# Optimization experiments

Hardware: AMD Instinct MI355X
Metric: run time of the kernel (lower is better)

## Reference

```python
import jax, jax.numpy as jnp
import numpy as np

D = 4096
H = 4 * D
EPS = 1e-5


def layer_norm(x, g, b):
    mu = jnp.mean(x, axis=-1, keepdims=True)
    var = jnp.mean(jnp.square(x - mu), axis=-1, keepdims=True)
    return (x - mu) * jax.lax.rsqrt(var + EPS) * g + b


def setup_inputs() -> dict:
    key = jax.random.key(0)
    ks = jax.random.split(key, 8)
    s = 0.02
    return {
        "x": jax.random.normal(ks[0], (2, 2048, D), dtype=jnp.float32),
        "Wq": jax.random.normal(ks[1], (D, D), dtype=jnp.float32) * s,
        "bq": jnp.zeros((D,), jnp.float32),
        "Wk": jax.random.normal(ks[2], (D, D), dtype=jnp.float32) * s,
        "bk": jnp.zeros((D,), jnp.float32),
        "Wv": jax.random.normal(ks[3], (D, D), dtype=jnp.float32) * s,
        "bv": jnp.zeros((D,), jnp.float32),
        "Wo": jax.random.normal(ks[4], (D, D), dtype=jnp.float32) * s,
        "bo": jnp.zeros((D,), jnp.float32),
        "g1": jnp.ones((D,), jnp.float32),
        "b1": jnp.zeros((D,), jnp.float32),
        "g2": jnp.ones((D,), jnp.float32),
        "b2": jnp.zeros((D,), jnp.float32),
        "W1": jax.random.normal(ks[5], (D, H), dtype=jnp.float32) * s,
        "bi1": jnp.zeros((H,), jnp.float32),
        "W2": jax.random.normal(ks[6], (H, D), dtype=jnp.float32) * s,
        "bi2": jnp.zeros((D,), jnp.float32),
    }


def reference(x, Wq, bq, Wk, bk, Wv, bv, Wo, bo, g1, b1, g2, b2, W1, bi1, W2, bi2):
    # single-head attention, scale = sqrt(D) (as in the source)
    Q = x @ Wq + bq          # [B, S, D]
    K = x @ Wk + bk
    V = x @ Wv + bv
    scores = jnp.einsum("bsd,btd->bst", Q, K) / jnp.sqrt(jnp.float32(D))
    attn = jax.nn.softmax(scores, axis=-1) @ V   # [B, S, D]
    x = attn @ Wo + bo + x
    x = layer_norm(x, g1, b1)
    h = jax.nn.gelu(x @ W1 + bi1, approximate=False)  # torch nn.GELU default = exact erf
    x = h @ W2 + bi2 + x
    x = layer_norm(x, g2, b2)
    return x
```

## Files before the change

kernel.cpp:

```cpp
#include <hip/hip_runtime.h>
#include <hip/hip_bf16.h>

typedef __bf16 bf16x8 __attribute__((ext_vector_type(8)));
typedef float  f32x4  __attribute__((ext_vector_type(4)));
typedef unsigned short u16;
typedef unsigned int   u32;

#define DEV __device__ __forceinline__

DEV u16 f2bu(float f){ union{float f; u32 i;} x; x.f=f; u32 r=x.i+0x7FFFu+((x.i>>16)&1u); return (u16)(r>>16); }
DEV u32 pack2(float a, float b){ return (u32)f2bu(a) | ((u32)f2bu(b)<<16); }

DEV void gload16(const u16* g, u16* l){
  __builtin_amdgcn_global_load_lds((const __attribute__((address_space(1))) void*)g,
                                   (__attribute__((address_space(3))) void*)l, 16, 0, 0);
}

template<int BIAS, int GELU, int RESF32, int OUTF32>
__global__ __launch_bounds__(512, 2) void gemm256(
    const u16* __restrict__ A, const u16* __restrict__ Bt,
    const float* __restrict__ bias, const float* __restrict__ resid,
    float* __restrict__ outF, u16* __restrict__ outB,
    int M, int N, int K, int SWZ,
    long long sA, long long sB, long long sC)
{
  __shared__ __align__(16) u16 As[4][8192];
  __shared__ __align__(16) u16 Bs[4][8192];

  const int tid  = threadIdx.x;
  const int lane = tid & 63;
  const int wave = tid >> 6;
  const int wm = wave >> 2;
  const int wn = wave & 3;

  int bx = blockIdx.x, by = blockIdx.y;
  if (SWZ) {
    const int gx = gridDim.x;
    const int nwg = gx * gridDim.y;
    const int flat = by * gx + bx;
    const int cpx = nwg >> 3;
    const int s = (flat & 7) * cpx + (flat >> 3);
    bx = s % gx; by = s / gx;
  }
  const int rowBase = by * 256;
  const int colBase = bx * 256;

  const u16* Ag = A + (size_t)blockIdx.z * sA + (size_t)rowBase * K;
  const u16* Bg = Bt + (size_t)blockIdx.z * sB + (size_t)colBase * K;

  const int qsw = (lane & 3) ^ ((lane >> 3) & 3);
  const u16* apA0 = Ag + (size_t)(wave*32 + (lane>>2)) * K + qsw*8;
  const u16* apA1 = apA0 + (size_t)16 * K;
  const u16* apB0 = Bg + (size_t)(wave*32 + (lane>>2)) * K + qsw*8;
  const u16* apB1 = apB0 + (size_t)16 * K;
  u16* dA0 = &As[0][wave*1024 + lane*8];
  u16* dA1 = dA0 + 512;
  u16* dB0 = &Bs[0][wave*1024 + lane*8];
  u16* dB1 = dB0 + 512;

#define STAGE(t) { const int _b = (t) & 3; const size_t _k = (size_t)(t) * 32;          \
    gload16(apA0 + _k, dA0 + _b*8192); gload16(apA1 + _k, dA1 + _b*8192);               \
    gload16(apB0 + _k, dB0 + _b*8192); gload16(apB1 + _k, dB1 + _b*8192); }

  const int r15 = lane & 15;
  const int gp  = (lane >> 4) ^ ((lane >> 1) & 3);
  const u16* rdA = &As[0][(wm*128 + r15)*32 + gp*8];
  const u16* rdB = &Bs[0][(wn*64  + r15)*32 + gp*8];

  f32x4 acc[8][4];
  const f32x4 fz = {0.f,0.f,0.f,0.f};
#pragma unroll
  for (int m=0;m<8;++m)
#pragma unroll
    for (int n=0;n<4;++n) acc[m][n] = fz;

  const int KT = K >> 5;
  STAGE(0);
  if (KT > 1) STAGE(1);
  if (KT > 2) STAGE(2);

  for (int t = 0; t < KT; ++t) {
    const int rem = KT - t;
    if (rem > 2)      asm volatile("s_waitcnt vmcnt(8)" ::: "memory");
    else if (rem > 1) asm volatile("s_waitcnt vmcnt(4)" ::: "memory");
    else              asm volatile("s_waitcnt vmcnt(0)" ::: "memory");
    __builtin_amdgcn_s_barrier();
    asm volatile("" ::: "memory");

    const u16* pa = rdA + (t & 3) * 8192;
    const u16* pb = rdB + (t & 3) * 8192;
    bf16x8 a[8], b[4];
#pragma unroll
    for (int m=0;m<8;++m) a[m] = *(const bf16x8*)(pa + m*512);
#pragma unroll
    for (int n=0;n<4;++n) b[n] = *(const bf16x8*)(pb + n*512);

    if (t + 3 < KT) STAGE(t + 3);

    __builtin_amdgcn_s_setprio(1);
#pragma unroll
    for (int m=0;m<8;++m)
#pragma unroll
      for (int n=0;n<4;++n)
        acc[m][n] = __builtin_amdgcn_mfma_f32_16x16x32_bf16(a[m], b[n], acc[m][n], 0,0,0);
    __builtin_amdgcn_s_setprio(0);
  }
#undef STAGE

  const long long cb = (long long)blockIdx.z * sC;
  const int q4 = (lane >> 4) * 4;
#pragma unroll
  for (int m=0;m<8;++m){
    const int row0 = rowBase + wm*128 + m*16 + q4;
#pragma unroll
    for (int n=0;n<4;++n){
      const int col = colBase + wn*64 + n*16 + r15;
      float bb = 0.f;
      if (BIAS) bb = bias[col];
#pragma unroll
      for (int r=0;r<4;++r){
        float v = acc[m][n][r] + bb;
        if (GELU) v = 0.5f*v*(1.f+erff(v*0.70710678118654752f));
        const size_t oi = (size_t)cb + (size_t)(row0+r)*N + col;
        if (RESF32) v += resid[oi];
        if (OUTF32) outF[oi] = v;
        else        outB[oi] = f2bu(v);
      }
    }
  }
}

__global__ __launch_bounds__(256) void tr_f32_bf16(
    const float* __restrict__ in, u16* __restrict__ out, int R, int C)
{
  __shared__ float tile[64][65];
  const int t = threadIdx.x;
  const int tr = blockIdx.y*64, tc = blockIdx.x*64;
  const int c4 = (t&15)*4;
#pragma unroll
  for (int i=0;i<4;++i){
    const int r = i*16 + (t>>4);
    const float4 v = *reinterpret_cast<const float4*>(&in[(size_t)(tr+r)*C + tc + c4]);
    tile[r][c4+0]=v.x; tile[r][c4+1]=v.y; tile[r][c4+2]=v.z; tile[r][c4+3]=v.w;
  }
  __syncthreads();
#pragma unroll
  for (int i=0;i<4;++i){
    const int c = i*16 + (t>>4);
    uint2 o;
    o.x = pack2(tile[c4+0][c], tile[c4+1][c]);
    o.y = pack2(tile[c4+2][c], tile[c4+3][c]);
    *reinterpret_cast<uint2*>(&out[(size_t)(tc+c)*R + tr + c4]) = o;
  }
}

__global__ __launch_bounds__(256) void tr_bf16(
    const u16* __restrict__ in, u16* __restrict__ out, int R, int C,
    long long sIn, long long sOut)
{
  __shared__ u16 tile[64][72];
  const long long z = blockIdx.z;
  in  += z*sIn; out += z*sOut;
  const int t = threadIdx.x;
  const int tr = blockIdx.y*64, tc = blockIdx.x*64;
  const int c4 = (t&15)*4;
#pragma unroll
  for (int i=0;i<4;++i){
    const int r = i*16 + (t>>4);
    const uint2 v = *reinterpret_cast<const uint2*>(&in[(size_t)(tr+r)*C + tc + c4]);
    tile[r][c4+0]=(u16)(v.x&0xffffu); tile[r][c4+1]=(u16)(v.x>>16);
    tile[r][c4+2]=(u16)(v.y&0xffffu); tile[r][c4+3]=(u16)(v.y>>16);
  }
  __syncthreads();
#pragma unroll
  for (int i=0;i<4;++i){
    const int c = i*16 + (t>>4);
    uint2 o;
    o.x = (u32)tile[c4+0][c] | ((u32)tile[c4+1][c]<<16);
    o.y = (u32)tile[c4+2][c] | ((u32)tile[c4+3][c]<<16);
    *reinterpret_cast<uint2*>(&out[(size_t)(tc+c)*R + tr + c4]) = o;
  }
}

__global__ __launch_bounds__(256) void cvt_f32_bf16(
    const float* __restrict__ in, u16* __restrict__ out, int n4)
{
  const int i = blockIdx.x*256 + threadIdx.x;
  if (i >= n4) return;
  const float4 v = reinterpret_cast<const float4*>(in)[i];
  uint2 o; o.x = pack2(v.x,v.y); o.y = pack2(v.z,v.w);
  reinterpret_cast<uint2*>(out)[i] = o;
}

__global__ __launch_bounds__(256) void softmax2048(
    const float* __restrict__ S, u16* __restrict__ P, float scale)
{
  const size_t row = blockIdx.x;
  const float4* src = reinterpret_cast<const float4*>(S + row*2048);
  const int t = threadIdx.x, lane = t&63, wave = t>>6;
  const float4 a = src[t], b = src[t+256];
  float v[8] = {a.x,a.y,a.z,a.w,b.x,b.y,b.z,b.w};
  float m = -3.4e38f;
#pragma unroll
  for (int i=0;i<8;++i){ v[i]*=scale; m = fmaxf(m, v[i]); }
#pragma unroll
  for (int o=32;o>0;o>>=1) m = fmaxf(m, __shfl_xor(m, o));
  __shared__ float red[8];
  if (lane==0) red[wave]=m;
  __syncthreads();
  m = fmaxf(fmaxf(red[0],red[1]), fmaxf(red[2],red[3]));
  float s = 0.f;
#pragma unroll
  for (int i=0;i<8;++i){ v[i] = __expf(v[i]-m); s += v[i]; }
#pragma unroll
  for (int o=32;o>0;o>>=1) s += __shfl_xor(s, o);
  if (lane==0) red[4+wave]=s;
  __syncthreads();
  s = red[4]+red[5]+red[6]+red[7];
  const float r = 1.f/s;
  uint2 o1, o2;
  o1.x = pack2(v[0]*r, v[1]*r); o1.y = pack2(v[2]*r, v[3]*r);
  o2.x = pack2(v[4]*r, v[5]*r); o2.y = pack2(v[6]*r, v[7]*r);
  uint2* dst = reinterpret_cast<uint2*>(P + row*2048);
  dst[t] = o1; dst[t+256] = o2;
}

template<int WB>
__global__ __launch_bounds__(256) void layernorm4096(
    const float* __restrict__ X, const float* __restrict__ g,
    const float* __restrict__ b, float* __restrict__ Yf, u16* __restrict__ Yb)
{
  const size_t row = blockIdx.x;
  const float4* src = reinterpret_cast<const float4*>(X + row*4096);
  const int t = threadIdx.x, lane = t&63, wave = t>>6;
  float4 xv[4];
  float sum=0.f, ss=0.f;
#pragma unroll
  for (int i=0;i<4;++i){
    xv[i] = src[t + 256*i];
    sum += xv[i].x+xv[i].y+xv[i].z+xv[i].w;
    ss  += xv[i].x*xv[i].x + xv[i].y*xv[i].y + xv[i].z*xv[i].z + xv[i].w*xv[i].w;
  }
#pragma unroll
  for (int o=32;o>0;o>>=1){ sum += __shfl_xor(sum,o); ss += __shfl_xor(ss,o); }
  __shared__ float rs[4], rq[4];
  if (lane==0){ rs[wave]=sum; rq[wave]=ss; }
  __syncthreads();
  sum = rs[0]+rs[1]+rs[2]+rs[3];
  ss  = rq[0]+rq[1]+rq[2]+rq[3];
  const float mean = sum * (1.f/4096.f);
  const float var  = ss * (1.f/4096.f) - mean*mean;
  const float rstd = rsqrtf(var + 1e-5f);
#pragma unroll
  for (int i=0;i<4;++i){
    const int i4 = t + 256*i;
    const float4 gv = reinterpret_cast<const float4*>(g)[i4];
    const float4 bvv = reinterpret_cast<const float4*>(b)[i4];
    float4 y;
    y.x = (xv[i].x-mean)*rstd*gv.x + bvv.x;
    y.y = (xv[i].y-mean)*rstd*gv.y + bvv.y;
    y.z = (xv[i].z-mean)*rstd*gv.z + bvv.z;
    y.w = (xv[i].w-mean)*rstd*gv.w + bvv.w;
    reinterpret_cast<float4*>(Yf + row*4096)[i4] = y;
    if (WB){
      uint2 o; o.x = pack2(y.x,y.y); o.y = pack2(y.z,y.w);
      reinterpret_cast<uint2*>(Yb + row*4096)[i4] = o;
    }
  }
}

extern "C" void kernel_launch(void* const* d_in, const int* in_sizes, int n_in,
                              void* d_out, int out_size, void* d_ws, size_t ws_size,
                              hipStream_t stream)
{
  constexpr int D = 4096, HD = 16384, S = 2048, B = 2;
  constexpr int NT = B*S;
  const float* x   = (const float*)d_in[0];
  const float* Wq  = (const float*)d_in[1];
  const float* bq  = (const float*)d_in[2];
  const float* Wk  = (const float*)d_in[3];
  const float* bk  = (const float*)d_in[4];
  const float* Wv  = (const float*)d_in[5];
  const float* bvp = (const float*)d_in[6];
  const float* Wo  = (const float*)d_in[7];
  const float* bo  = (const float*)d_in[8];
  const float* g1  = (const float*)d_in[9];
  const float* b1  = (const float*)d_in[10];
  const float* g2  = (const float*)d_in[11];
  const float* b2  = (const float*)d_in[12];
  const float* W1  = (const float*)d_in[13];
  const float* bi1 = (const float*)d_in[14];
  const float* W2  = (const float*)d_in[15];
  const float* bi2 = (const float*)d_in[16];

  char* ws = (char*)d_ws;
  const size_t MB32 = 33554432;
  u16* WqT = (u16*)(ws + 0*MB32);
  u16* WkT = (u16*)(ws + 1*MB32);
  u16* WvT = (u16*)(ws + 2*MB32);
  u16* WoT = (u16*)(ws + 3*MB32);
  u16* W1T = (u16*)(ws + 0*MB32);
  u16* xb  = (u16*)(ws + 4*MB32);
  u16* Qb  = (u16*)(ws + 5*MB32);
  u16* Kb  = (u16*)(ws + 6*MB32);
  u16* Vb  = (u16*)(ws + 7*MB32);
  u16* W2T = (u16*)(ws + 4*MB32);
  u16* Vt  = (u16*)(ws + 8*MB32);
  float* scoresF = (float*)(ws + 9*MB32);
  u16* Pb  = (u16*)(ws + 10*MB32);
  u16* Ab  = (u16*)(ws + 10*MB32 + 16777216);
  u16* hB  = (u16*)(ws + 8*MB32);
  float* x1raw = (float*)(ws + 12*MB32);
  float* x2raw = (float*)(ws + 12*MB32);
  float* x1f   = (float*)(ws + 14*MB32);
  u16*   x1b   = (u16*)(ws + 16*MB32);

  const dim3 blk(256), blkG(512);
  const long long SD = (long long)S*D, SS = (long long)S*S, DS = (long long)D*S;

  tr_f32_bf16<<<dim3(D/64, D/64), blk, 0, stream>>>(Wq, WqT, D, D);
  tr_f32_bf16<<<dim3(D/64, D/64), blk, 0, stream>>>(Wk, WkT, D, D);
  tr_f32_bf16<<<dim3(D/64, D/64), blk, 0, stream>>>(Wv, WvT, D, D);
  tr_f32_bf16<<<dim3(D/64, D/64), blk, 0, stream>>>(Wo, WoT, D, D);
  cvt_f32_bf16<<<dim3((NT*D/4)/256), blk, 0, stream>>>(x, xb, NT*D/4);

  gemm256<1,0,0,0><<<dim3(D/256, NT/256, 1), blkG, 0, stream>>>(xb, WqT, bq,  nullptr, nullptr, Qb, NT, D, D, 1, 0,0,0);
  gemm256<1,0,0,0><<<dim3(D/256, NT/256, 1), blkG, 0, stream>>>(xb, WkT, bk,  nullptr, nullptr, Kb, NT, D, D, 1, 0,0,0);
  gemm256<1,0,0,0><<<dim3(D/256, NT/256, 1), blkG, 0, stream>>>(xb, WvT, bvp, nullptr, nullptr, Vb, NT, D, D, 1, 0,0,0);
  tr_bf16<<<dim3(D/64, S/64, B), blk, 0, stream>>>(Vb, Vt, S, D, SD, SD);

  gemm256<0,0,0,1><<<dim3(S/256, S/256, B), blkG, 0, stream>>>(Qb, Kb, nullptr, nullptr, scoresF, nullptr, S, S, D, 0, SD, SD, SS);
  softmax2048<<<dim3(B*S), blk, 0, stream>>>(scoresF, Pb, 0.015625f);
  gemm256<0,0,0,0><<<dim3(D/256, S/256, B), blkG, 0, stream>>>(Pb, Vt, nullptr, nullptr, nullptr, Ab, S, D, S, 0, SS, DS, SD);

  gemm256<1,0,1,1><<<dim3(D/256, NT/256, 1), blkG, 0, stream>>>(Ab, WoT, bo, x, x1raw, nullptr, NT, D, D, 1, 0,0,0);
  layernorm4096<1><<<dim3(NT), blk, 0, stream>>>(x1raw, g1, b1, x1f, x1b);

  tr_f32_bf16<<<dim3(HD/64, D/64), blk, 0, stream>>>(W1, W1T, D, HD);
  gemm256<1,1,0,0><<<dim3(HD/256, NT/256, 1), blkG, 0, stream>>>(x1b, W1T, bi1, nullptr, nullptr, hB, NT, HD, D, 1, 0,0,0);
  tr_f32_bf16<<<dim3(D/64, HD/64), blk, 0, stream>>>(W2, W2T, HD, D);
  gemm256<1,0,1,1><<<dim3(D/256, NT/256, 1), blkG, 0, stream>>>(hB, W2T, bi2, x1f, x2raw, nullptr, NT, D, HD, 1, 0,0,0);
  layernorm4096<0><<<dim3(NT), blk, 0, stream>>>(x2raw, g2, b2, (float*)d_out, nullptr);
}
```

Measured before the change: 2.165 ms.

## Split GEMM k-step into two half-tile phases and remap block swizzle

Each k-iteration of the 256x256 GEMM now runs as two phases: half the A fragments are loaded, the A prefetch is issued, and 16 MFMAs run; then the other half of A is loaded, the B prefetch is issued, and the second 16 MFMAs run. Extra barriers and lgkmcnt waits are placed between phases so LDS reads and global-to-LDS copies interleave with matrix math, and fewer A registers are live at once. The block swizzle is replaced by a fixed mapping into 16x16 tile groups, intended to improve L2 reuse. That mapping hardcodes 16 rows and a 256-block group size, so it is only correct for grids shaped like NT=4096, and the added barriers may cost more than the overlap gains.

```diff
diff --git a/kernel.cpp b/kernel.cpp
--- a/kernel.cpp
+++ b/kernel.cpp
@@ -34,13 +34,13 @@
   const int wn = wave & 3;
 
   int bx = blockIdx.x, by = blockIdx.y;
-  if (SWZ) {
+  if (SWZ == 2) {
     const int gx = gridDim.x;
-    const int nwg = gx * gridDim.y;
-    const int flat = by * gx + bx;
-    const int cpx = nwg >> 3;
-    const int s = (flat & 7) * cpx + (flat >> 3);
-    bx = s % gx; by = s / gx;
+    const int f  = by * gx + bx;
+    const int g  = f >> 8, r = f & 255;
+    const int u  = (r & 7) | ((r >> 7) << 3);
+    bx = g * 16 + u;
+    by = (r >> 3) & 15;
   }
   const int rowBase = by * 256;
   const int colBase = bx * 256;
@@ -58,8 +58,9 @@
   u16* dB0 = &Bs[0][wave*1024 + lane*8];
   u16* dB1 = dB0 + 512;
 
-#define STAGE(t) { const int _b = (t) & 3; const size_t _k = (size_t)(t) * 32;          \
-    gload16(apA0 + _k, dA0 + _b*8192); gload16(apA1 + _k, dA1 + _b*8192);               \
+#define STAGE_A(t) { const int _b = (t) & 3; const size_t _k = (size_t)(t) * 32;        \
+    gload16(apA0 + _k, dA0 + _b*8192); gload16(apA1 + _k, dA1 + _b*8192); }
+#define STAGE_B(t) { const int _b = (t) & 3; const size_t _k = (size_t)(t) * 32;        \
     gload16(apB0 + _k, dB0 + _b*8192); gload16(apB1 + _k, dB1 + _b*8192); }
 
   const int r15 = lane & 15;
@@ -75,37 +76,57 @@
     for (int n=0;n<4;++n) acc[m][n] = fz;
 
   const int KT = K >> 5;
-  STAGE(0);
-  if (KT > 1) STAGE(1);
-  if (KT > 2) STAGE(2);
+  STAGE_A(0); STAGE_B(0);
+  if (KT > 1) { STAGE_A(1); STAGE_B(1); }
+  if (KT > 2) { STAGE_A(2); STAGE_B(2); }
+  if (KT > 2)      asm volatile("s_waitcnt vmcnt(8)" ::: "memory");
+  else if (KT > 1) asm volatile("s_waitcnt vmcnt(4)" ::: "memory");
+  else             asm volatile("s_waitcnt vmcnt(0)" ::: "memory");
+  __builtin_amdgcn_s_barrier();
+  asm volatile("" ::: "memory");
 
   for (int t = 0; t < KT; ++t) {
-    const int rem = KT - t;
-    if (rem > 2)      asm volatile("s_waitcnt vmcnt(8)" ::: "memory");
-    else if (rem > 1) asm volatile("s_waitcnt vmcnt(4)" ::: "memory");
-    else              asm volatile("s_waitcnt vmcnt(0)" ::: "memory");
-    __builtin_amdgcn_s_barrier();
-    asm volatile("" ::: "memory");
-
     const u16* pa = rdA + (t & 3) * 8192;
     const u16* pb = rdB + (t & 3) * 8192;
-    bf16x8 a[8], b[4];
-#pragma unroll
-    for (int m=0;m<8;++m) a[m] = *(const bf16x8*)(pa + m*512);
-#pragma unroll
-    for (int n=0;n<4;++n) b[n] = *(const bf16x8*)(pb + n*512);
-
-    if (t + 3 < KT) STAGE(t + 3);
-
+    bf16x8 a[4], b[4];
+#pragma unroll
+    for (int i=0;i<4;++i) a[i] = *(const bf16x8*)(pa + i*512);
+#pragma unroll
+    for (int i=0;i<4;++i) b[i] = *(const bf16x8*)(pb + i*512);
+    if (t + 3 < KT) STAGE_A(t + 3);
+    asm volatile("" ::: "memory");
+    __builtin_amdgcn_s_barrier();
+    asm volatile("s_waitcnt lgkmcnt(0)" ::: "memory");
+    __builtin_amdgcn_sched_barrier(0);
     __builtin_amdgcn_s_setprio(1);
 #pragma unroll
-    for (int m=0;m<8;++m)
+    for (int m=0;m<4;++m)
 #pragma unroll
       for (int n=0;n<4;++n)
         acc[m][n] = __builtin_amdgcn_mfma_f32_16x16x32_bf16(a[m], b[n], acc[m][n], 0,0,0);
     __builtin_amdgcn_s_setprio(0);
-  }
-#undef STAGE
+    asm volatile("" ::: "memory");
+    __builtin_amdgcn_s_barrier();
+#pragma unroll
+    for (int i=0;i<4;++i) a[i] = *(const bf16x8*)(pa + (i+4)*512);
+    if (t + 3 < KT) STAGE_B(t + 3);
+    if (t + 3 < KT)      asm volatile("s_waitcnt vmcnt(8)" ::: "memory");
+    else if (t + 2 < KT) asm volatile("s_waitcnt vmcnt(4)" ::: "memory");
+    else if (t + 1 < KT) asm volatile("s_waitcnt vmcnt(0)" ::: "memory");
+    asm volatile("" ::: "memory");
+    __builtin_amdgcn_s_barrier();
+    asm volatile("s_waitcnt lgkmcnt(0)" ::: "memory");
+    __builtin_amdgcn_sched_barrier(0);
+    __builtin_amdgcn_s_setprio(1);
+#pragma unroll
+    for (int m=0;m<4;++m)
+#pragma unroll
+      for (int n=0;n<4;++n)
+        acc[m+4][n] = __builtin_amdgcn_mfma_f32_16x16x32_bf16(a[m], b[n], acc[m+4][n], 0,0,0);
+    __builtin_amdgcn_s_setprio(0);
+  }
+#undef STAGE_A
+#undef STAGE_B
 
   const long long cb = (long long)blockIdx.z * sC;
   const int q4 = (lane >> 4) * 4;
@@ -324,21 +345,21 @@
   tr_f32_bf16<<<dim3(D/64, D/64), blk, 0, stream>>>(Wo, WoT, D, D);
   cvt_f32_bf16<<<dim3((NT*D/4)/256), blk, 0, stream>>>(x, xb, NT*D/4);
 
-  gemm256<1,0,0,0><<<dim3(D/256, NT/256, 1), blkG, 0, stream>>>(xb, WqT, bq,  nullptr, nullptr, Qb, NT, D, D, 1, 0,0,0);
-  gemm256<1,0,0,0><<<dim3(D/256, NT/256, 1), blkG, 0, stream>>>(xb, WkT, bk,  nullptr, nullptr, Kb, NT, D, D, 1, 0,0,0);
-  gemm256<1,0,0,0><<<dim3(D/256, NT/256, 1), blkG, 0, stream>>>(xb, WvT, bvp, nullptr, nullptr, Vb, NT, D, D, 1, 0,0,0);
+  gemm256<1,0,0,0><<<dim3(D/256, NT/256, 1), blkG, 0, stream>>>(xb, WqT, bq,  nullptr, nullptr, Qb, NT, D, D, 2, 0,0,0);
+  gemm256<1,0,0,0><<<dim3(D/256, NT/256, 1), blkG, 0, stream>>>(xb, WkT, bk,  nullptr, nullptr, Kb, NT, D, D, 2, 0,0,0);
+  gemm256<1,0,0,0><<<dim3(D/256, NT/256, 1), blkG, 0, stream>>>(xb, WvT, bvp, nullptr, nullptr, Vb, NT, D, D, 2, 0,0,0);
   tr_bf16<<<dim3(D/64, S/64, B), blk, 0, stream>>>(Vb, Vt, S, D, SD, SD);
 
   gemm256<0,0,0,1><<<dim3(S/256, S/256, B), blkG, 0, stream>>>(Qb, Kb, nullptr, nullptr, scoresF, nullptr, S, S, D, 0, SD, SD, SS);
   softmax2048<<<dim3(B*S), blk, 0, stream>>>(scoresF, Pb, 0.015625f);
   gemm256<0,0,0,0><<<dim3(D/256, S/256, B), blkG, 0, stream>>>(Pb, Vt, nullptr, nullptr, nullptr, Ab, S, D, S, 0, SS, DS, SD);
 
-  gemm256<1,0,1,1><<<dim3(D/256, NT/256, 1), blkG, 0, stream>>>(Ab, WoT, bo, x, x1raw, nullptr, NT, D, D, 1, 0,0,0);
+  gemm256<1,0,1,1><<<dim3(D/256, NT/256, 1), blkG, 0, stream>>>(Ab, WoT, bo, x, x1raw, nullptr, NT, D, D, 2, 0,0,0);
   layernorm4096<1><<<dim3(NT), blk, 0, stream>>>(x1raw, g1, b1, x1f, x1b);
 
   tr_f32_bf16<<<dim3(HD/64, D/64), blk, 0, stream>>>(W1, W1T, D, HD);
-  gemm256<1,1,0,0><<<dim3(HD/256, NT/256, 1), blkG, 0, stream>>>(x1b, W1T, bi1, nullptr, nullptr, hB, NT, HD, D, 1, 0,0,0);
+  gemm256<1,1,0,0><<<dim3(HD/256, NT/256, 1), blkG, 0, stream>>>(x1b, W1T, bi1, nullptr, nullptr, hB, NT, HD, D, 2, 0,0,0);
   tr_f32_bf16<<<dim3(D/64, HD/64), blk, 0, stream>>>(W2, W2T, HD, D);
-  gemm256<1,0,1,1><<<dim3(D/256, NT/256, 1), blkG, 0, stream>>>(hB, W2T, bi2, x1f, x2raw, nullptr, NT, D, HD, 1, 0,0,0);
+  gemm256<1,0,1,1><<<dim3(D/256, NT/256, 1), blkG, 0, stream>>>(hB, W2T, bi2, x1f, x2raw, nullptr, NT, D, HD, 2, 0,0,0);
   layernorm4096<0><<<dim3(NT), blk, 0, stream>>>(x2raw, g2, b2, (float*)d_out, nullptr);
 }
```

Result: slower. 2.381 ms (+10.0%).
